# Performance work log

Hardware: AMD Instinct MI355X
Metric: run time of the kernel (lower is better)

Reference implementation:

```python
import math
import jax, jax.numpy as jnp
import numpy as np

B, S, HID = 1, 2048, 2048
H, D = 32, 64            # heads, head_dim = HID // H
THETA = 10000.0
EPS = 1e-6
LAYER_IDX = 12
LAM_INIT = 0.8 - 0.6 * math.exp(-0.3 * LAYER_IDX)  # lambda_init_fn(layer_idx)
SCALE = 1.0 / math.sqrt(D)


def _rope_cos_sin(seq_len, dim):
    inv_freq = 1.0 / (THETA ** (np.arange(0, dim, 2, dtype=np.float64) / dim))
    freqs = np.outer(np.arange(seq_len, dtype=np.float64), inv_freq)
    emb = np.concatenate([freqs, freqs], axis=-1)  # [S, D] (llama duplicates freqs)
    return jnp.asarray(np.cos(emb), jnp.float32), jnp.asarray(np.sin(emb), jnp.float32)


def _rotate_half(x):
    return jnp.concatenate([-x[..., D // 2:], x[..., : D // 2]], axis=-1)


def _apply_rope(x, cos, sin):
    # x: [B, H, S, D]; cos/sin: [S, D] broadcast over B, H
    return x * cos + _rotate_half(x) * sin


def setup_inputs() -> dict:
    key = jax.random.key(0)
    ks = jax.random.split(key, 10)
    return {
        "hidden_states": jax.random.normal(ks[0], (B, S, HID), jnp.float32),
        "Wq": jax.random.normal(ks[1], (2 * HID, HID), jnp.float32) * 0.02,
        "Wk": jax.random.normal(ks[2], (2 * HID, HID), jnp.float32) * 0.02,
        "Wv": jax.random.normal(ks[3], (HID, HID), jnp.float32) * 0.02,
        "Wo": jax.random.normal(ks[4], (HID, HID), jnp.float32) * 0.02,
        "lambda_q1": jax.random.normal(ks[5], (D,), jnp.float32) * 0.1,
        "lambda_k1": jax.random.normal(ks[6], (D,), jnp.float32) * 0.1,
        "lambda_q2": jax.random.normal(ks[7], (D,), jnp.float32) * 0.1,
        "lambda_k2": jax.random.normal(ks[8], (D,), jnp.float32) * 0.1,
        "subln_w": jnp.ones((D,), jnp.float32),
    }


def reference(hidden_states, Wq, Wk, Wv, Wo,
              lambda_q1, lambda_k1, lambda_q2, lambda_k2, subln_w):
    # Projections (nn.Linear, no bias): x @ W.T
    q = hidden_states @ Wq.T                       # [B, S, 2*HID]
    k = hidden_states @ Wk.T                       # [B, S, 2*HID]
    v = hidden_states @ Wv.T                       # [B, S, HID]

    def to_heads(t):  # [B, S, H*D] -> [B, H, S, D]
        return t.reshape(B, S, H, D).transpose(0, 2, 1, 3)

    q1, q2 = jnp.split(q, 2, axis=-1)
    k1, k2 = jnp.split(k, 2, axis=-1)
    q1, q2, k1, k2, v = map(to_heads, (q1, q2, k1, k2, v))

    cos, sin = _rope_cos_sin(S, D)
    q1, k1 = _apply_rope(q1, cos, sin), _apply_rope(k1, cos, sin)
    q2, k2 = _apply_rope(q2, cos, sin), _apply_rope(k2, cos, sin)

    # Causal additive mask [S, S]
    causal = jnp.tril(jnp.ones((S, S), bool))
    neg_inf = jnp.finfo(jnp.float32).min
    mask = jnp.where(causal, 0.0, neg_inf)

    s1 = jnp.einsum("bhqd,bhkd->bhqk", q1, k1) * SCALE + mask
    s2 = jnp.einsum("bhqd,bhkd->bhqk", q2, k2) * SCALE + mask

    lam = (jnp.exp(jnp.sum(lambda_q1 * lambda_k1))
           - jnp.exp(jnp.sum(lambda_q2 * lambda_k2)) + LAM_INIT)

    attn_w = jax.nn.softmax(s1, axis=-1) - lam * jax.nn.softmax(s2, axis=-1)
    attn = jnp.einsum("bhqk,bhkd->bhqd", attn_w, v)  # [B, H, S, D]

    # Head-wise RMSNorm (LlamaRMSNorm over value_head_dim)
    var = jnp.mean(jnp.square(attn), axis=-1, keepdims=True)
    attn = attn * jax.lax.rsqrt(var + EPS) * subln_w
    attn = attn * (1.0 - LAM_INIT)

    out = attn.transpose(0, 2, 1, 3).reshape(B, S, HID) @ Wo.T
    return out
```

## Files before the change

### kernel.cpp

```cpp
#include <hip/hip_runtime.h>


typedef __bf16 bf16;
typedef __bf16 bf16x4 __attribute__((ext_vector_type(4)));
typedef __bf16 bf16x8 __attribute__((ext_vector_type(8)));
typedef float  f32x4  __attribute__((ext_vector_type(4)));
typedef unsigned int u32;
typedef u32 u32x2 __attribute__((ext_vector_type(2)));
typedef u32 u32x4 __attribute__((ext_vector_type(4)));

#define MFMA(a, b, c) __builtin_amdgcn_mfma_f32_16x16x32_bf16((a), (b), (c), 0, 0, 0)

#define S_LEN   2048
#define HID_DIM 2048
#define NHEAD   32
#define HD      64
#define QKV_N   10240
#define LAM_INIT 0.7836057665316245f
#define ONE_MINUS_LAM_INIT 0.21639423346837553f
#define QSCALE  0.18033688011112042f
#define RMS_EPS 1e-6f
#define L2T     0.4152410118609203f

__device__ __forceinline__ void gld16(const void* g, void* l) {
    __builtin_amdgcn_global_load_lds(
        (const __attribute__((address_space(1))) void*)g,
        (__attribute__((address_space(3))) void*)l, 16, 0, 0);
}

__device__ __forceinline__ void pa_build(u32 x, u32 y, int quad, u32& wlo, u32& whi) {
#if __has_builtin(__builtin_amdgcn_permlane32_swap) && __has_builtin(__builtin_amdgcn_permlane16_swap)
    u32x2 s = __builtin_amdgcn_permlane32_swap(x, y, false, false);
    u32x2 t = __builtin_amdgcn_permlane16_swap(s.x, s.y, false, false);
    wlo = t.x;
    whi = t.y;
#else
    const u32 x16 = (u32)__shfl_xor((int)x, 16, 64);
    const u32 x32 = (u32)__shfl_xor((int)x, 32, 64);
    const u32 x48 = (u32)__shfl_xor((int)x, 48, 64);
    const u32 y16 = (u32)__shfl_xor((int)y, 16, 64);
    const u32 y32 = (u32)__shfl_xor((int)y, 32, 64);
    const u32 y48 = (u32)__shfl_xor((int)y, 48, 64);
    wlo = (quad == 0) ? x   : (quad == 1) ? x48 : (quad == 2) ? y32 : y16;
    whi = (quad == 0) ? x16 : (quad == 1) ? x32 : (quad == 2) ? y48 : y;
#endif
}

__global__ void cvt_all(const float* __restrict__ hs, const float* __restrict__ Wq,
                        const float* __restrict__ Wk, const float* __restrict__ Wv,
                        const float* __restrict__ Wo,
                        const float* __restrict__ lq1, const float* __restrict__ lk1,
                        const float* __restrict__ lq2, const float* __restrict__ lk2,
                        bf16* __restrict__ hsb, bf16* __restrict__ Wb,
                        bf16* __restrict__ Wob, float* __restrict__ lam_out) {
    const int bid = blockIdx.x;
    if (bid >= 28672) {
        const int t = threadIdx.x;
        if (t < 64) {
            float a = lq1[t] * lk1[t];
            float b = lq2[t] * lk2[t];
            #pragma unroll
            for (int off = 32; off > 0; off >>= 1) {
                a += __shfl_xor(a, off, 64);
                b += __shfl_xor(b, off, 64);
            }
            if (t == 0) lam_out[0] = expf(a) - expf(b) + LAM_INIT;
        }
        return;
    }
    const float* src; bf16* dst; int off;
    if      (bid <  4096) { src = hs; dst = hsb;            off = bid;         }
    else if (bid < 12288) { src = Wq; dst = Wb;             off = bid - 4096;  }
    else if (bid < 20480) { src = Wk; dst = Wb +  8388608;  off = bid - 12288; }
    else if (bid < 24576) { src = Wv; dst = Wb + 16777216;  off = bid - 20480; }
    else                  { src = Wo; dst = Wob;            off = bid - 24576; }
    const int i = off * 1024 + threadIdx.x * 4;
    float4 v = *(const float4*)(src + i);
    bf16x4 o = { (bf16)v.x, (bf16)v.y, (bf16)v.z, (bf16)v.w };
    *(bf16x4*)(dst + i) = o;
}

__global__ __launch_bounds__(256, 3)
void qkv_rope_gemm(const bf16* __restrict__ A, const bf16* __restrict__ B,
                   bf16* __restrict__ Q1, bf16* __restrict__ Q2,
                   bf16* __restrict__ K1, bf16* __restrict__ K2,
                   bf16* __restrict__ Vt) {
    __shared__ __align__(16) bf16 As[128 * 64];
    __shared__ __align__(16) bf16 Bs[128 * 64];
    const int tid  = threadIdx.x;
    const int wave = tid >> 6, lane = tid & 63;
    const int wm = wave >> 1, wn = wave & 1;
    const int l = lane & 15, quad = lane >> 4;
    const int m0 = blockIdx.y * 128, n0 = blockIdx.x * 128;

    f32x4 acc[4][4];
    #pragma unroll
    for (int i = 0; i < 4; ++i)
        #pragma unroll
        for (int j = 0; j < 4; ++j) acc[i][j] = (f32x4){0.f, 0.f, 0.f, 0.f};

    const int rr  = tid >> 3;
    const int csw = ((tid & 7) ^ (rr & 7)) * 8;
    const bf16* Ag = A + (size_t)(m0 + rr) * HID_DIM + csw;
    const bf16* Bg = B + (size_t)(n0 + rr) * HID_DIM + csw;

    for (int kt = 0; kt < HID_DIM; kt += 64) {
        __syncthreads();
        #pragma unroll
        for (int j = 0; j < 4; ++j) {
            gld16(Ag + (size_t)(32 * j) * HID_DIM + kt, As + j * 2048 + tid * 8);
            gld16(Bg + (size_t)(32 * j) * HID_DIM + kt, Bs + j * 2048 + tid * 8);
        }
        __syncthreads();

        #pragma unroll
        for (int ks = 0; ks < 2; ++ks) {
            const int co = (((ks << 2) | quad) ^ (l & 7)) << 3;
            bf16x8 hf[4], wf[4];
            #pragma unroll
            for (int hi = 0; hi < 4; ++hi)
                hf[hi] = *(const bf16x8*)(As + (wm * 64 + hi * 16 + l) * 64 + co);
            #pragma unroll
            for (int wi = 0; wi < 4; ++wi)
                wf[wi] = *(const bf16x8*)(Bs + (wn * 64 + wi * 16 + l) * 64 + co);
            #pragma unroll
            for (int wi = 0; wi < 4; ++wi)
                #pragma unroll
                for (int hi = 0; hi < 4; ++hi)
                    acc[wi][hi] = MFMA(wf[wi], hf[hi], acc[wi][hi]);
        }
    }

    const int c = n0 + wn * 64;
    const int sbase = m0 + wm * 64;
    bf16* dst; int off; float scale = 1.0f; bool isv = false;
    if      (c < 2048) { dst = Q1; off = c;        scale = QSCALE; }
    else if (c < 4096) { dst = Q2; off = c - 2048; scale = QSCALE; }
    else if (c < 6144) { dst = K1; off = c - 4096; }
    else if (c < 8192) { dst = K2; off = c - 6144; }
    else               { isv = true; off = c - 8192; }
    const int h = off >> 6;

    if (!isv) {
        float invf[2][4];
        #pragma unroll
        for (int p = 0; p < 2; ++p)
            #pragma unroll
            for (int r = 0; r < 4; ++r)
                invf[p][r] = exp2f(-(float)(p * 16 + quad * 4 + r) * L2T);

        #pragma unroll
        for (int hi = 0; hi < 4; ++hi) {
            const float s = (float)(sbase + hi * 16 + l);
            float cs[2][4], sn[2][4];
            #pragma unroll
            for (int p = 0; p < 2; ++p)
                #pragma unroll
                for (int r = 0; r < 4; ++r) {
                    const float ang = s * invf[p][r];
                    cs[p][r] = __cosf(ang);
                    sn[p][r] = __sinf(ang);
                }
            bf16* rowp = dst + ((size_t)h * S_LEN + sbase + hi * 16 + l) * HD + quad * 4;
            #pragma unroll
            for (int wi = 0; wi < 4; ++wi) {
                const int p = wi & 1;
                const float sign = (wi < 2) ? -1.0f : 1.0f;
                bf16x4 o;
                #pragma unroll
                for (int r = 0; r < 4; ++r)
                    o[r] = (bf16)((acc[wi][hi][r] * cs[p][r] +
                                   sign * acc[wi ^ 2][hi][r] * sn[p][r]) * scale);
                *(bf16x4*)(rowp + wi * 16) = o;
            }
        }
    } else {
        #pragma unroll
        for (int wi = 0; wi < 4; ++wi)
            #pragma unroll
            for (int r = 0; r < 4; ++r) {
                bf16* vrow = Vt + ((size_t)h * HD + wi * 16 + quad * 4 + r) * S_LEN + sbase;
                #pragma unroll
                for (int hi = 0; hi < 4; ++hi)
                    vrow[hi * 16 + l] = (bf16)acc[wi][hi][r];
            }
    }
}

__global__ __launch_bounds__(256, 3)
void gemm_bt_splitk(const bf16* __restrict__ A, const bf16* __restrict__ B,
                    float* __restrict__ Cout, int M, int N, int K_total, int K_part) {
    __shared__ __align__(16) bf16 As[128 * 64];
    __shared__ __align__(16) bf16 Bs[128 * 64];
    const int tid  = threadIdx.x;
    const int wave = tid >> 6, lane = tid & 63;
    const int wm = wave >> 1, wn = wave & 1;
    const int l = lane & 15, quad = lane >> 4;
    const int m0 = blockIdx.y * 128, n0 = blockIdx.x * 128;
    const int kz = blockIdx.z * K_part;

    f32x4 acc[4][4];
    #pragma unroll
    for (int i = 0; i < 4; ++i)
        #pragma unroll
        for (int j = 0; j < 4; ++j) acc[i][j] = (f32x4){0.f, 0.f, 0.f, 0.f};

    const int rr  = tid >> 3;
    const int csw = ((tid & 7) ^ (rr & 7)) * 8;
    const bf16* Ag = A + (size_t)(m0 + rr) * K_total + kz + csw;
    const bf16* Bg = B + (size_t)(n0 + rr) * K_total + kz + csw;

    for (int kt = 0; kt < K_part; kt += 64) {
        __syncthreads();
        #pragma unroll
        for (int j = 0; j < 4; ++j) {
            gld16(Ag + (size_t)(32 * j) * K_total + kt, As + j * 2048 + tid * 8);
            gld16(Bg + (size_t)(32 * j) * K_total + kt, Bs + j * 2048 + tid * 8);
        }
        __syncthreads();

        #pragma unroll
        for (int ks = 0; ks < 2; ++ks) {
            const int co = (((ks << 2) | quad) ^ (l & 7)) << 3;
            bf16x8 af[4], bfr[4];
            #pragma unroll
            for (int mi = 0; mi < 4; ++mi)
                af[mi] = *(const bf16x8*)(As + (wm * 64 + mi * 16 + l) * 64 + co);
            #pragma unroll
            for (int ni = 0; ni < 4; ++ni)
                bfr[ni] = *(const bf16x8*)(Bs + (wn * 64 + ni * 16 + l) * 64 + co);
            #pragma unroll
            for (int mi = 0; mi < 4; ++mi)
                #pragma unroll
                for (int ni = 0; ni < 4; ++ni)
                    acc[mi][ni] = MFMA(af[mi], bfr[ni], acc[mi][ni]);
        }
    }

    float* Pf = Cout + (size_t)blockIdx.z * M * N;
    #pragma unroll
    for (int mi = 0; mi < 4; ++mi)
        #pragma unroll
        for (int ni = 0; ni < 4; ++ni)
            #pragma unroll
            for (int r = 0; r < 4; ++r) {
                const int row = m0 + wm * 64 + mi * 16 + quad * 4 + r;
                const int col = n0 + wn * 64 + ni * 16 + l;
                Pf[(size_t)row * N + col] = acc[mi][ni][r];
            }
}

__global__ void reduce_add(const float* __restrict__ p, float* __restrict__ out, int n) {
    const int i = (blockIdx.x * 256 + threadIdx.x) * 4;
    float4 a = *(const float4*)(p + i);
    float4 b = *(const float4*)(p + n + i);
    float4 o = { a.x + b.x, a.y + b.y, a.z + b.z, a.w + b.w };
    *(float4*)(out + i) = o;
}

__global__ __launch_bounds__(256, 2)
void diff_attn(const bf16* __restrict__ Q1, const bf16* __restrict__ K1,
               const bf16* __restrict__ Q2, const bf16* __restrict__ K2,
               const bf16* __restrict__ Vt, const float* __restrict__ lam_p,
               const float* __restrict__ subln_w, bf16* __restrict__ attn_out) {
    const int bid  = blockIdx.x;
    const int h    = (bid >> 1) & 31;
    const int idx  = bid >> 6;
    const int qb   = (bid & 1) ? idx : (15 - idx);
    const int q0   = qb * 128;
    const int tid  = threadIdx.x;
    const int wave = tid >> 6, lane = tid & 63;
    const int sid  = wave >> 1, half = wave & 1;
    const int l    = lane & 15, quad = lane >> 4;
    const int q0w  = q0 + half * 64;

    __shared__ __align__(16) char smem[49152];

    const bf16* Qh  = (sid ? Q2 : Q1) + ((size_t)h * S_LEN + q0w) * HD;
    const bf16* K1g = K1 + (size_t)h * S_LEN * HD;
    const bf16* K2g = K2 + (size_t)h * S_LEN * HD;
    const bf16* Vtg = Vt + (size_t)h * HD * S_LEN;

    const int rr  = tid >> 3;
    const int csw = ((tid & 7) ^ (rr & 7)) * 8;
    const int sw8 = l & 7;

    auto stage = [&](int kv, int bufb) {
        const bf16* k1p = K1g + (size_t)(kv + rr) * HD + csw;
        const bf16* k2p = K2g + (size_t)(kv + rr) * HD + csw;
        const bf16* vtp = Vtg + (size_t)rr * S_LEN + kv + csw;
        bf16* d1 = (bf16*)(smem + bufb)         + tid * 8;
        bf16* d2 = (bf16*)(smem + bufb + 8192)  + tid * 8;
        bf16* dv = (bf16*)(smem + bufb + 16384) + tid * 8;
        gld16(k1p,                       d1);
        gld16(k1p + (size_t)32 * HD,     d1 + 2048);
        gld16(k2p,                       d2);
        gld16(k2p + (size_t)32 * HD,     d2 + 2048);
        gld16(vtp,                       dv);
        gld16(vtp + (size_t)32 * S_LEN,  dv + 2048);
    };

    bf16x8 qf[4][2];
    #pragma unroll
    for (int g = 0; g < 4; ++g)
        #pragma unroll
        for (int ks = 0; ks < 2; ++ks)
            qf[g][ks] = *(const bf16x8*)(Qh + (g * 16 + l) * HD + ks * 32 + quad * 8);

    f32x4 O[4][4];
    #pragma unroll
    for (int g = 0; g < 4; ++g)
        #pragma unroll
        for (int nd = 0; nd < 4; ++nd)
            O[g][nd] = (f32x4){0.f, 0.f, 0.f, 0.f};
    float csum[4] = {0.f, 0.f, 0.f, 0.f};

    const int T = 2 * qb + 2;

    stage(0, 0);
    asm volatile("s_waitcnt vmcnt(0)" ::: "memory");
    __builtin_amdgcn_s_barrier();

    for (int t = 0; t < T; ++t) {
        const int kv0 = t * 64;
        const int bb  = (t & 1) * 24576;

        if (t + 1 < T) stage(kv0 + 64, 24576 - bb);

        if (kv0 <= q0w) {
            const bool diag = (kv0 == q0w);
            const bf16* Ksm = (const bf16*)(smem + bb + (sid ? 8192 : 0));
            const bf16* Vts = (const bf16*)(smem + bb + 16384);

            bf16x8 ka[4][2];
            #pragma unroll
            for (int mk = 0; mk < 4; ++mk) {
                const int krow = (mk * 16 + l) * 64;
                ka[mk][0] = *(const bf16x8*)(Ksm + krow + ((quad ^ sw8) << 3));
                ka[mk][1] = *(const bf16x8*)(Ksm + krow + (((4 + quad) ^ sw8) << 3));
            }
            bf16x8 vb[2][4];
            #pragma unroll
            for (int ks = 0; ks < 2; ++ks)
                #pragma unroll
                for (int nd = 0; nd < 4; ++nd)
                    vb[ks][nd] = *(const bf16x8*)(Vts + (nd * 16 + l) * 64 +
                                                  ((((ks << 2) + quad) ^ sw8) << 3));

            __builtin_amdgcn_s_setprio(1);
            #pragma unroll
            for (int g = 0; g < 4; ++g) {
                f32x4 c[4];
                #pragma unroll
                for (int mk = 0; mk < 4; ++mk) {
                    c[mk] = (f32x4){0.f, 0.f, 0.f, 0.f};
                    c[mk] = MFMA(ka[mk][0], qf[g][0], c[mk]);
                    c[mk] = MFMA(ka[mk][1], qf[g][1], c[mk]);
                }
                u32 dw[4][2];
                float lsum = 0.f;
                #pragma unroll
                for (int mk = 0; mk < 4; ++mk) {
                    float p[4];
                    #pragma unroll
                    for (int r = 0; r < 4; ++r) {
                        p[r] = __builtin_amdgcn_exp2f(c[mk][r]);
                        if (diag && (mk * 16 + quad * 4 + r > g * 16 + l)) p[r] = 0.f;
                        lsum += p[r];
                    }
                    asm("v_cvt_pk_bf16_f32 %0, %1, %2" : "=v"(dw[mk][0]) : "v"(p[0]), "v"(p[1]));
                    asm("v_cvt_pk_bf16_f32 %0, %1, %2" : "=v"(dw[mk][1]) : "v"(p[2]), "v"(p[3]));
                }
                csum[g] += lsum;

                u32 wa0, wa1, wa2, wa3, wb0, wb1, wb2, wb3;
                pa_build(dw[0][0], dw[1][0], quad, wa0, wa2);
                pa_build(dw[0][1], dw[1][1], quad, wa1, wa3);
                pa_build(dw[2][0], dw[3][0], quad, wb0, wb2);
                pa_build(dw[2][1], dw[3][1], quad, wb1, wb3);
                u32x4 w0 = {wa0, wa1, wa2, wa3};
                u32x4 w1 = {wb0, wb1, wb2, wb3};
                bf16x8 pa0, pa1;
                __builtin_memcpy(&pa0, &w0, 16);
                __builtin_memcpy(&pa1, &w1, 16);

                #pragma unroll
                for (int nd = 0; nd < 4; ++nd) {
                    O[g][nd] = MFMA(pa0, vb[0][nd], O[g][nd]);
                    O[g][nd] = MFMA(pa1, vb[1][nd], O[g][nd]);
                }
            }
            __builtin_amdgcn_s_setprio(0);
        }

        asm volatile("s_waitcnt vmcnt(0)" ::: "memory");
        __builtin_amdgcn_s_barrier();
    }

    __syncthreads();
    float* epi = (float*)(smem + half * 16640);

    #pragma unroll
    for (int g = 0; g < 4; ++g) {
        csum[g] += __shfl_xor(csum[g], 16, 64);
        csum[g] += __shfl_xor(csum[g], 32, 64);
    }

    if (sid == 1) {
        const float lam = lam_p[0];
        #pragma unroll
        for (int mi = 0; mi < 4; ++mi)
            #pragma unroll
            for (int r = 0; r < 4; ++r) {
                const float inv = lam / __shfl(csum[mi], quad * 4 + r, 64);
                const int row = mi * 16 + quad * 4 + r;
                #pragma unroll
                for (int ni = 0; ni < 4; ++ni)
                    epi[row * 65 + ni * 16 + l] = O[mi][ni][r] * inv;
            }
    }
    __syncthreads();

    if (sid == 0) {
        float sw[4];
        #pragma unroll
        for (int ni = 0; ni < 4; ++ni) sw[ni] = subln_w[ni * 16 + l];

        #pragma unroll
        for (int mi = 0; mi < 4; ++mi) {
            float inv1[4];
            #pragma unroll
            for (int r = 0; r < 4; ++r)
                inv1[r] = 1.0f / __shfl(csum[mi], quad * 4 + r, 64);

            float v[4][4]; float ssq[4] = {0.f, 0.f, 0.f, 0.f};
            #pragma unroll
            for (int ni = 0; ni < 4; ++ni)
                #pragma unroll
                for (int r = 0; r < 4; ++r) {
                    const int row = mi * 16 + quad * 4 + r;
                    const float x = O[mi][ni][r] * inv1[r] - epi[row * 65 + ni * 16 + l];
                    v[ni][r] = x;
                    ssq[r] += x * x;
                }
            #pragma unroll
            for (int r = 0; r < 4; ++r) {
                float s = ssq[r];
                s += __shfl_xor(s, 1, 64);
                s += __shfl_xor(s, 2, 64);
                s += __shfl_xor(s, 4, 64);
                s += __shfl_xor(s, 8, 64);
                ssq[r] = rsqrtf(s * (1.0f / 64.0f) + RMS_EPS) * ONE_MINUS_LAM_INIT;
            }
            #pragma unroll
            for (int ni = 0; ni < 4; ++ni)
                #pragma unroll
                for (int r = 0; r < 4; ++r) {
                    const int row = q0w + mi * 16 + quad * 4 + r;
                    attn_out[(size_t)row * HID_DIM + h * 64 + ni * 16 + l] =
                        (bf16)(v[ni][r] * ssq[r] * sw[ni]);
                }
        }
    }
}

extern "C" void kernel_launch(void* const* d_in, const int* in_sizes, int n_in,
                              void* d_out, int out_size, void* d_ws, size_t ws_size,
                              hipStream_t stream) {
    const float* hs  = (const float*)d_in[0];
    const float* Wq  = (const float*)d_in[1];
    const float* Wk  = (const float*)d_in[2];
    const float* Wv  = (const float*)d_in[3];
    const float* Wo  = (const float*)d_in[4];
    const float* lq1 = (const float*)d_in[5];
    const float* lk1 = (const float*)d_in[6];
    const float* lq2 = (const float*)d_in[7];
    const float* lk2 = (const float*)d_in[8];
    const float* slw = (const float*)d_in[9];

    if (ws_size < 151000000u) return;

    char* ws = (char*)d_ws;
    bf16*  hsb  = (bf16*)(ws);
    bf16*  Wb   = (bf16*)(ws + 8388608);
    bf16*  Wob  = (bf16*)(ws + 50331648);
    float* part = (float*)(ws + 58720256);
    bf16*  Q1b  = (bf16*)(ws + 100663296);
    bf16*  K1b  = (bf16*)(ws + 109051904);
    bf16*  Q2b  = (bf16*)(ws + 117440512);
    bf16*  K2b  = (bf16*)(ws + 125829120);
    bf16*  Vtb  = (bf16*)(ws + 134217728);
    bf16*  abuf = (bf16*)(ws + 142606336);
    float* lamp = (float*)(ws + 150994944);

    cvt_all<<<28673, 256, 0, stream>>>(hs, Wq, Wk, Wv, Wo, lq1, lk1, lq2, lk2,
                                       hsb, Wb, Wob, lamp);

    qkv_rope_gemm<<<dim3(QKV_N / 128, S_LEN / 128), 256, 0, stream>>>(
        hsb, Wb, Q1b, Q2b, K1b, K2b, Vtb);

    diff_attn<<<512, 256, 0, stream>>>(Q1b, K1b, Q2b, K2b, Vtb, lamp, slw, abuf);

    gemm_bt_splitk<<<dim3(HID_DIM / 128, S_LEN / 128, 2), 256, 0, stream>>>(
        abuf, Wob, part, S_LEN, HID_DIM, HID_DIM, HID_DIM / 2);
    reduce_add<<<4096, 256, 0, stream>>>(part, (float*)d_out, S_LEN * HID_DIM);
}
```

Measured before the change: 359.0 us.

## Split attention KV tiles across waves with smaller query blocks; widen conversion stores

```diff
diff --git a/kernel.cpp b/kernel.cpp
--- a/kernel.cpp
+++ b/kernel.cpp
@@ -54,7 +54,7 @@
                         bf16* __restrict__ hsb, bf16* __restrict__ Wb,
                         bf16* __restrict__ Wob, float* __restrict__ lam_out) {
     const int bid = blockIdx.x;
-    if (bid >= 28672) {
+    if (bid >= 14336) {
         const int t = threadIdx.x;
         if (t < 64) {
             float a = lq1[t] * lk1[t];
@@ -69,18 +69,20 @@
         return;
     }
     const float* src; bf16* dst; int off;
-    if      (bid <  4096) { src = hs; dst = hsb;            off = bid;         }
-    else if (bid < 12288) { src = Wq; dst = Wb;             off = bid - 4096;  }
-    else if (bid < 20480) { src = Wk; dst = Wb +  8388608;  off = bid - 12288; }
-    else if (bid < 24576) { src = Wv; dst = Wb + 16777216;  off = bid - 20480; }
-    else                  { src = Wo; dst = Wob;            off = bid - 24576; }
-    const int i = off * 1024 + threadIdx.x * 4;
-    float4 v = *(const float4*)(src + i);
-    bf16x4 o = { (bf16)v.x, (bf16)v.y, (bf16)v.z, (bf16)v.w };
-    *(bf16x4*)(dst + i) = o;
-}
-
-__global__ __launch_bounds__(256, 3)
+    if      (bid <  2048) { src = hs; dst = hsb;            off = bid;         }
+    else if (bid <  6144) { src = Wq; dst = Wb;             off = bid - 2048;  }
+    else if (bid < 10240) { src = Wk; dst = Wb +  8388608;  off = bid - 6144;  }
+    else if (bid < 12288) { src = Wv; dst = Wb + 16777216;  off = bid - 10240; }
+    else                  { src = Wo; dst = Wob;            off = bid - 12288; }
+    const int i = off * 2048 + threadIdx.x * 8;
+    float4 a = *(const float4*)(src + i);
+    float4 b = *(const float4*)(src + i + 4);
+    bf16x8 o = { (bf16)a.x, (bf16)a.y, (bf16)a.z, (bf16)a.w,
+                 (bf16)b.x, (bf16)b.y, (bf16)b.z, (bf16)b.w };
+    *(bf16x8*)(dst + i) = o;
+}
+
+__global__ __launch_bounds__(256, 4)
 void qkv_rope_gemm(const bf16* __restrict__ A, const bf16* __restrict__ B,
                    bf16* __restrict__ Q1, bf16* __restrict__ Q2,
                    bf16* __restrict__ K1, bf16* __restrict__ K2,
@@ -187,7 +189,7 @@
     }
 }
 
-__global__ __launch_bounds__(256, 3)
+__global__ __launch_bounds__(256, 4)
 void gemm_bt_splitk(const bf16* __restrict__ A, const bf16* __restrict__ B,
                     float* __restrict__ Cout, int M, int N, int K_total, int K_part) {
     __shared__ __align__(16) bf16 As[128 * 64];
@@ -258,25 +260,24 @@
     *(float4*)(out + i) = o;
 }
 
-__global__ __launch_bounds__(256, 2)
+__global__ __launch_bounds__(256, 3)
 void diff_attn(const bf16* __restrict__ Q1, const bf16* __restrict__ K1,
                const bf16* __restrict__ Q2, const bf16* __restrict__ K2,
                const bf16* __restrict__ Vt, const float* __restrict__ lam_p,
                const float* __restrict__ subln_w, bf16* __restrict__ attn_out) {
-    const int bid  = blockIdx.x;
-    const int h    = (bid >> 1) & 31;
-    const int idx  = bid >> 6;
-    const int qb   = (bid & 1) ? idx : (15 - idx);
-    const int q0   = qb * 128;
+    const int bid   = blockIdx.x;
+    const int h     = (bid >> 1) & 31;
+    const int qpair = bid >> 6;
+    const int qb    = (bid & 1) ? qpair : (31 - qpair);
+    const int q0    = qb * 64;
     const int tid  = threadIdx.x;
     const int wave = tid >> 6, lane = tid & 63;
-    const int sid  = wave >> 1, half = wave & 1;
+    const int sid  = wave >> 1, ks = wave & 1;
     const int l    = lane & 15, quad = lane >> 4;
-    const int q0w  = q0 + half * 64;
 
     __shared__ __align__(16) char smem[49152];
 
-    const bf16* Qh  = (sid ? Q2 : Q1) + ((size_t)h * S_LEN + q0w) * HD;
+    const bf16* Qh  = (sid ? Q2 : Q1) + ((size_t)h * S_LEN + q0) * HD;
     const bf16* K1g = K1 + (size_t)h * S_LEN * HD;
     const bf16* K2g = K2 + (size_t)h * S_LEN * HD;
     const bf16* Vtg = Vt + (size_t)h * HD * S_LEN;
@@ -304,8 +305,8 @@
     #pragma unroll
     for (int g = 0; g < 4; ++g)
         #pragma unroll
-        for (int ks = 0; ks < 2; ++ks)
-            qf[g][ks] = *(const bf16x8*)(Qh + (g * 16 + l) * HD + ks * 32 + quad * 8);
+        for (int dh = 0; dh < 2; ++dh)
+            qf[g][dh] = *(const bf16x8*)(Qh + (g * 16 + l) * HD + dh * 32 + quad * 8);
 
     f32x4 O[4][4];
     #pragma unroll
@@ -315,57 +316,54 @@
             O[g][nd] = (f32x4){0.f, 0.f, 0.f, 0.f};
     float csum[4] = {0.f, 0.f, 0.f, 0.f};
 
-    const int T = 2 * qb + 2;
+    const int T = qb + 1;
 
     stage(0, 0);
     asm volatile("s_waitcnt vmcnt(0)" ::: "memory");
     __builtin_amdgcn_s_barrier();
 
     for (int t = 0; t < T; ++t) {
-        const int kv0 = t * 64;
-        const int bb  = (t & 1) * 24576;
-
-        if (t + 1 < T) stage(kv0 + 64, 24576 - bb);
-
-        if (kv0 <= q0w) {
-            const bool diag = (kv0 == q0w);
+        const int bb = (t & 1) * 24576;
+        if (t + 1 < T) stage((t + 1) * 64, 24576 - bb);
+
+        {
+            const bool diag = (t == qb);
             const bf16* Ksm = (const bf16*)(smem + bb + (sid ? 8192 : 0));
             const bf16* Vts = (const bf16*)(smem + bb + 16384);
 
-            bf16x8 ka[4][2];
-            #pragma unroll
-            for (int mk = 0; mk < 4; ++mk) {
-                const int krow = (mk * 16 + l) * 64;
+            bf16x8 ka[2][2];
+            #pragma unroll
+            for (int mk = 0; mk < 2; ++mk) {
+                const int krow = ((2 * ks + mk) * 16 + l) * 64;
                 ka[mk][0] = *(const bf16x8*)(Ksm + krow + ((quad ^ sw8) << 3));
                 ka[mk][1] = *(const bf16x8*)(Ksm + krow + (((4 + quad) ^ sw8) << 3));
             }
-            bf16x8 vb[2][4];
-            #pragma unroll
-            for (int ks = 0; ks < 2; ++ks)
-                #pragma unroll
-                for (int nd = 0; nd < 4; ++nd)
-                    vb[ks][nd] = *(const bf16x8*)(Vts + (nd * 16 + l) * 64 +
-                                                  ((((ks << 2) + quad) ^ sw8) << 3));
+            bf16x8 vb[4];
+            #pragma unroll
+            for (int nd = 0; nd < 4; ++nd)
+                vb[nd] = *(const bf16x8*)(Vts + (nd * 16 + l) * 64 +
+                                          ((((ks << 2) + quad) ^ sw8) << 3));
 
             __builtin_amdgcn_s_setprio(1);
             #pragma unroll
             for (int g = 0; g < 4; ++g) {
-                f32x4 c[4];
-                #pragma unroll
-                for (int mk = 0; mk < 4; ++mk) {
+                f32x4 c[2];
+                #pragma unroll
+                for (int mk = 0; mk < 2; ++mk) {
                     c[mk] = (f32x4){0.f, 0.f, 0.f, 0.f};
                     c[mk] = MFMA(ka[mk][0], qf[g][0], c[mk]);
                     c[mk] = MFMA(ka[mk][1], qf[g][1], c[mk]);
                 }
-                u32 dw[4][2];
+                u32 dw[2][2];
                 float lsum = 0.f;
                 #pragma unroll
-                for (int mk = 0; mk < 4; ++mk) {
+                for (int mk = 0; mk < 2; ++mk) {
                     float p[4];
                     #pragma unroll
                     for (int r = 0; r < 4; ++r) {
                         p[r] = __builtin_amdgcn_exp2f(c[mk][r]);
-                        if (diag && (mk * 16 + quad * 4 + r > g * 16 + l)) p[r] = 0.f;
+                        if (diag && ((2 * ks + mk) * 16 + quad * 4 + r > g * 16 + l))
+                            p[r] = 0.f;
                         lsum += p[r];
                     }
                     asm("v_cvt_pk_bf16_f32 %0, %1, %2" : "=v"(dw[mk][0]) : "v"(p[0]), "v"(p[1]));
@@ -373,22 +371,16 @@
                 }
                 csum[g] += lsum;
 
-                u32 wa0, wa1, wa2, wa3, wb0, wb1, wb2, wb3;
-                pa_build(dw[0][0], dw[1][0], quad, wa0, wa2);
-                pa_build(dw[0][1], dw[1][1], quad, wa1, wa3);
-                pa_build(dw[2][0], dw[3][0], quad, wb0, wb2);
-                pa_build(dw[2][1], dw[3][1], quad, wb1, wb3);
-                u32x4 w0 = {wa0, wa1, wa2, wa3};
-                u32x4 w1 = {wb0, wb1, wb2, wb3};
-                bf16x8 pa0, pa1;
-                __builtin_memcpy(&pa0, &w0, 16);
-                __builtin_memcpy(&pa1, &w1, 16);
-
-                #pragma unroll
-                for (int nd = 0; nd < 4; ++nd) {
-                    O[g][nd] = MFMA(pa0, vb[0][nd], O[g][nd]);
-                    O[g][nd] = MFMA(pa1, vb[1][nd], O[g][nd]);
-                }
+                u32 w0, w1, w2, w3;
+                pa_build(dw[0][0], dw[1][0], quad, w0, w2);
+                pa_build(dw[0][1], dw[1][1], quad, w1, w3);
+                u32x4 wv = {w0, w1, w2, w3};
+                bf16x8 pa;
+                __builtin_memcpy(&pa, &wv, 16);
+
+                #pragma unroll
+                for (int nd = 0; nd < 4; ++nd)
+                    O[g][nd] = MFMA(pa, vb[nd], O[g][nd]);
             }
             __builtin_amdgcn_s_setprio(0);
         }
@@ -398,15 +390,40 @@
     }
 
     __syncthreads();
-    float* epi = (float*)(smem + half * 16640);
+    float* dO = (float*)(smem + sid * 17408);
+    float* dC = (float*)(smem + 34816 + sid * 1024);
+    if (ks == 1) {
+        #pragma unroll
+        for (int g = 0; g < 4; ++g)
+            #pragma unroll
+            for (int nd = 0; nd < 4; ++nd)
+                *(f32x4*)(dO + lane * 68 + (g * 4 + nd) * 4) = O[g][nd];
+        #pragma unroll
+        for (int g = 0; g < 4; ++g) dC[g * 64 + lane] = csum[g];
+    }
+    __syncthreads();
+    if (ks == 0) {
+        #pragma unroll
+        for (int g = 0; g < 4; ++g) {
+            #pragma unroll
+            for (int nd = 0; nd < 4; ++nd) {
+                f32x4 o = *(const f32x4*)(dO + lane * 68 + (g * 4 + nd) * 4);
+                O[g][nd] += o;
+            }
+            csum[g] += dC[g * 64 + lane];
+        }
+    }
 
     #pragma unroll
     for (int g = 0; g < 4; ++g) {
         csum[g] += __shfl_xor(csum[g], 16, 64);
         csum[g] += __shfl_xor(csum[g], 32, 64);
     }
-
-    if (sid == 1) {
+    __syncthreads();
+
+    float* epi = (float*)smem;
+
+    if (sid == 1 && ks == 0) {
         const float lam = lam_p[0];
         #pragma unroll
         for (int mi = 0; mi < 4; ++mi)
@@ -421,7 +438,7 @@
     }
     __syncthreads();
 
-    if (sid == 0) {
+    if (sid == 0 && ks == 0) {
         float sw[4];
         #pragma unroll
         for (int ni = 0; ni < 4; ++ni) sw[ni] = subln_w[ni * 16 + l];
@@ -456,7 +473,7 @@
             for (int ni = 0; ni < 4; ++ni)
                 #pragma unroll
                 for (int r = 0; r < 4; ++r) {
-                    const int row = q0w + mi * 16 + quad * 4 + r;
+                    const int row = q0 + mi * 16 + quad * 4 + r;
                     attn_out[(size_t)row * HID_DIM + h * 64 + ni * 16 + l] =
                         (bf16)(v[ni][r] * ssq[r] * sw[ni]);
                 }
@@ -493,13 +510,13 @@
     bf16*  abuf = (bf16*)(ws + 142606336);
     float* lamp = (float*)(ws + 150994944);
 
-    cvt_all<<<28673, 256, 0, stream>>>(hs, Wq, Wk, Wv, Wo, lq1, lk1, lq2, lk2,
+    cvt_all<<<14337, 256, 0, stream>>>(hs, Wq, Wk, Wv, Wo, lq1, lk1, lq2, lk2,
                                        hsb, Wb, Wob, lamp);
 
     qkv_rope_gemm<<<dim3(QKV_N / 128, S_LEN / 128), 256, 0, stream>>>(
         hsb, Wb, Q1b, Q2b, K1b, K2b, Vtb);
 
-    diff_attn<<<512, 256, 0, stream>>>(Q1b, K1b, Q2b, K2b, Vtb, lamp, slw, abuf);
+    diff_attn<<<1024, 256, 0, stream>>>(Q1b, K1b, Q2b, K2b, Vtb, lamp, slw, abuf);
 
     gemm_bt_splitk<<<dim3(HID_DIM / 128, S_LEN / 128, 2), 256, 0, stream>>>(
         abuf, Wob, part, S_LEN, HID_DIM, HID_DIM, HID_DIM / 2);
```

New measurement: 384.1 us. +7.0%, slower.
